# Performance work log

Measured on AMD Instinct MI355X. Metric: run time of the kernel, lower is better.

## Reference

```python
import jax, jax.numpy as jnp
import numpy as np
from jax import lax

# Model dims (match init_kwargs config)
HID = 2048      # hidden_size
NH = 64         # num_heads
P = 64          # head_dim
N = 128         # ssm_state_size
G = 1           # n_groups
CS = 256        # chunk_size
K = 4           # conv kernel
D_INNER = NH * P                  # 4096
CONV_DIM = D_INNER + 2 * G * N    # 4352
PROJ = D_INNER + CONV_DIM + NH    # 8512
EPS = 1e-5
BATCH, SEQ = 2, 2048


def setup_inputs() -> dict:
    key = jax.random.key(0)
    ks = jax.random.split(key, 8)
    hidden_states = jax.random.normal(ks[0], (BATCH, SEQ, HID), dtype=jnp.float32)
    W_in = jax.random.normal(ks[1], (PROJ, HID), dtype=jnp.float32) * 0.02
    conv_w = jax.random.normal(ks[2], (CONV_DIM, 1, K), dtype=jnp.float32) * 0.2
    conv_b = jax.random.normal(ks[3], (CONV_DIM,), dtype=jnp.float32) * 0.02
    # dt_bias initialized like inv-softplus of dt in [1e-3, 1e-1]
    dt = jnp.exp(jax.random.uniform(ks[4], (NH,)) * (np.log(0.1) - np.log(0.001)) + np.log(0.001))
    dt_bias = (dt + jnp.log(-jnp.expm1(-dt))).astype(jnp.float32)
    A_log = jnp.log(jnp.arange(1, NH + 1, dtype=jnp.float32))
    D_param = jnp.ones((NH,), dtype=jnp.float32)
    norm_w = jnp.ones((D_INNER,), dtype=jnp.float32)
    W_out = jax.random.normal(ks[5], (HID, D_INNER), dtype=jnp.float32) * 0.02
    return {"hidden_states": hidden_states, "W_in": W_in, "conv_w": conv_w,
            "conv_b": conv_b, "dt_bias": dt_bias, "A_log": A_log,
            "D_param": D_param, "norm_w": norm_w, "W_out": W_out}


def _segsum(x):
    # x: (..., c) -> (..., c, c); seg[i, j] = sum_{j < k <= i} x_k (diag 0), -inf above diag
    T = x.shape[-1]
    xc = jnp.cumsum(x, axis=-1)
    seg = xc[..., :, None] - xc[..., None, :]
    mask = jnp.tril(jnp.ones((T, T), dtype=bool))
    return jnp.where(mask, seg, -jnp.inf)


def _mamba2_forward(hidden_states, W_in, conv_w, conv_b, dt_bias, A_log, D_param, norm_w, W_out):
    B_, L_ = hidden_states.shape[:2]
    proj = hidden_states @ W_in.T                           # (b, l, PROJ)
    z = proj[..., :D_INNER]                                 # gate
    xBC = proj[..., D_INNER:D_INNER + CONV_DIM]
    dt = proj[..., D_INNER + CONV_DIM:]                     # (b, l, NH)

    # depthwise causal conv1d + silu
    xc = lax.conv_general_dilated(
        jnp.transpose(xBC, (0, 2, 1)), conv_w,
        window_strides=(1,), padding=[(K - 1, 0)],
        feature_group_count=CONV_DIM)                        # (b, CONV_DIM, l)
    xc = xc + conv_b[None, :, None]
    xBC = jax.nn.silu(jnp.transpose(xc, (0, 2, 1)))          # (b, l, CONV_DIM)

    x = xBC[..., :D_INNER].reshape(B_, L_, NH, P)
    Bm = xBC[..., D_INNER:D_INNER + G * N].reshape(B_, L_, G, N)
    Cm = xBC[..., D_INNER + G * N:].reshape(B_, L_, G, N)

    dt = jax.nn.softplus(dt + dt_bias)                       # (b, l, NH)
    A = -jnp.exp(A_log)                                      # (NH,)

    Bh = jnp.repeat(Bm, NH // G, axis=2)                     # (b, l, h, n)
    Ch = jnp.repeat(Cm, NH // G, axis=2)

    # ---- chunked SSD scan ----
    nc = L_ // CS
    x_dt = (x * dt[..., None]).reshape(B_, nc, CS, NH, P)    # (b, c, s, h, p)
    B_c = Bh.reshape(B_, nc, CS, NH, N)
    C_c = Ch.reshape(B_, nc, CS, NH, N)
    dA = jnp.transpose((dt * A).reshape(B_, nc, CS, NH), (0, 3, 1, 2))  # (b, h, c, s)
    A_cum = jnp.cumsum(dA, axis=-1)                          # (b, h, c, s)

    Lmat = jnp.exp(_segsum(dA))                              # (b, h, c, s, s)
    Y_diag = jnp.einsum('bclhn,bcshn,bhcls,bcshp->bclhp', C_c, B_c, Lmat, x_dt)

    decay_states = jnp.exp(A_cum[..., -1:] - A_cum)          # (b, h, c, s)
    states = jnp.einsum('bclhn,bhcl,bclhp->bchpn', B_c, decay_states, x_dt)

    da_last = A_cum[..., -1]                                 # (b, h, c)

    def step(prev, inp):
        s_k, d_k = inp                                       # (b,h,p,n), (b,h)
        new = prev * jnp.exp(d_k)[..., None, None] + s_k
        return new, prev

    _, prev_states = lax.scan(step, jnp.zeros((B_, NH, P, N), dtype=x.dtype),
                              (jnp.transpose(states, (1, 0, 2, 3, 4)),
                               jnp.transpose(da_last, (2, 0, 1))))
    prev_states = jnp.transpose(prev_states, (1, 2, 0, 3, 4))  # (b, h, c, p, n)

    Y_off = jnp.einsum('bclhn,bhcpn,bhcl->bclhp', C_c, prev_states, jnp.exp(A_cum))

    y = (Y_diag + Y_off).reshape(B_, L_, NH, P) + D_param[None, None, :, None] * x
    y = y.reshape(B_, L_, D_INNER)

    # gated grouped RMSNorm (norm_before_gate=False): norm(y * silu(z)) * w
    g = y * jax.nn.silu(z)
    gs = D_INNER // G
    gr = g.reshape(B_, L_, G, gs)
    var = jnp.mean(gr * gr, axis=-1, keepdims=True)
    gn = (gr * lax.rsqrt(var + EPS)).reshape(B_, L_, D_INNER) * norm_w

    return gn @ W_out.T                                      # (b, l, HID)


def reference(hidden_states, W_in, conv_w, conv_b, dt_bias, A_log, D_param, norm_w, W_out):
    return _mamba2_forward(hidden_states, W_in, conv_w, conv_b, dt_bias, A_log, D_param, norm_w, W_out)
```

## Files before the change

### kernel.cpp

```cpp
#include <hip/hip_runtime.h>

#define SEQLEN 2048
#define NHEADS 64
#define PDIM 64
#define NSTATE 128
#define CSIZE 256
#define NCHUNK 8
#define DINNER 4096
#define CONVD 4352
#define PROJD 8512

using s8v = __attribute__((ext_vector_type(8))) short;
using f4v = __attribute__((ext_vector_type(4))) float;
using bf8v = __attribute__((ext_vector_type(8))) __bf16;

__device__ __forceinline__ short f2bf(float x) {
  union { float f; unsigned u; } t; t.f = x;
  unsigned r = t.u + 0x7FFFu + ((t.u >> 16) & 1u);
  return (short)(r >> 16);
}
__device__ __forceinline__ float bf2f(short s) {
  union { unsigned u; float f; } t;
  t.u = ((unsigned)(unsigned short)s) << 16;
  return t.f;
}

__device__ __forceinline__ f4v mfma_bf16(s8v a, s8v b, f4v c) {
  return __builtin_amdgcn_mfma_f32_16x16x32_bf16(
      __builtin_bit_cast(bf8v, a), __builtin_bit_cast(bf8v, b), c, 0, 0, 0);
}

__device__ __forceinline__ void gll16(const void* g, void* l) {
  __builtin_amdgcn_global_load_lds(
      (const __attribute__((address_space(1))) unsigned*)g,
      (__attribute__((address_space(3))) unsigned*)l, 16, 0, 0);
}

__global__ __launch_bounds__(256) void cast_bf16_kernel(
    const float* __restrict__ in, short* __restrict__ out, int n4) {
  int i = blockIdx.x * 256 + threadIdx.x;
  if (i < n4) {
    float4 v = ((const float4*)in)[i];
    short4 o;
    o.x = f2bf(v.x); o.y = f2bf(v.y); o.z = f2bf(v.z); o.w = f2bf(v.w);
    ((short4*)out)[i] = o;
  }
}

__global__ __launch_bounds__(256, 4) void gemm1_kernel(
    const short* __restrict__ A, const short* __restrict__ B,
    short* __restrict__ z, short* __restrict__ xbc, float* __restrict__ dtb) {
  const int K = 2048;
  const int bid = blockIdx.x;
  const int panel = bid / (67 * 4), rem = bid % (67 * 4);
  const int bx = rem >> 2, by = panel * 4 + (rem & 3);
  const int tn0 = bx * 128, tm0 = by * 128;
  __shared__ alignas(16) short lds[8704];
  short* As = lds;
  short* Bs = lds + 4096;
  short* Cs = lds;
  const int tid = threadIdx.x;
  const int lane = tid & 63, wid = tid >> 6;
  const int wm = (wid >> 1) * 64, wn = (wid & 1) * 64;
  const int lr = lane & 15, q = lane >> 4;
  const int fA = (lr & 3) ^ ((lr >> 2) & 3);
  const int qs = (q ^ fA) * 8;
  f4v acc[4][4];
  for (int i = 0; i < 4; i++)
    for (int j = 0; j < 4; j++)
      for (int r = 0; r < 4; r++) acc[i][j][r] = 0.f;

  for (int k0 = 0; k0 < K; k0 += 32) {
    __syncthreads();
    for (int it = 0; it < 2; it++) {
      int ci = it * 256 + tid;
      int row = ci >> 2;
      int cg = ((ci & 3) ^ (row & 3) ^ ((row >> 2) & 3)) << 3;
      gll16(&A[(size_t)(tm0 + row) * K + k0 + cg], &As[ci * 8]);
      gll16(&B[(size_t)(tn0 + row) * K + k0 + cg], &Bs[ci * 8]);
    }
    __syncthreads();
    s8v af[4], bfr[4];
    for (int i = 0; i < 4; i++) af[i]  = *(const s8v*)&As[(wm + i * 16 + lr) * 32 + qs];
    for (int j = 0; j < 4; j++) bfr[j] = *(const s8v*)&Bs[(wn + j * 16 + lr) * 32 + qs];
    for (int i = 0; i < 4; i++)
      for (int j = 0; j < 4; j++)
        acc[i][j] = mfma_bf16(af[i], bfr[j], acc[i][j]);
  }
  __syncthreads();

  if (tn0 < 8448) {
    short* outp; int rowstride, colbase;
    if (tn0 < DINNER) { outp = z;   rowstride = DINNER; colbase = tn0; }
    else              { outp = xbc; rowstride = CONVD;  colbase = tn0 - DINNER; }
    for (int hh = 0; hh < 2; hh++) {
      if ((wid >> 1) == hh) {
        for (int i = 0; i < 4; i++)
          for (int j = 0; j < 4; j++)
            for (int r = 0; r < 4; r++)
              Cs[(i * 16 + q * 4 + r) * 136 + wn + j * 16 + lr] = f2bf(acc[i][j][r]);
      }
      __syncthreads();
      for (int ps = 0; ps < 4; ps++) {
        int idx = ps * 256 + tid;
        int r = idx >> 4, c8 = (idx & 15) * 8;
        s8v v = *(const s8v*)&Cs[r * 136 + c8];
        *(s8v*)&outp[(size_t)(tm0 + hh * 64 + r) * rowstride + colbase + c8] = v;
      }
      __syncthreads();
    }
  } else {
    for (int i = 0; i < 4; i++)
      for (int j = 0; j < 4; j++) {
        int c0 = tn0 + wn + j * 16 + lr;
        if (c0 < PROJD)
          for (int r = 0; r < 4; r++)
            dtb[(size_t)(tm0 + wm + i * 16 + q * 4 + r) * NHEADS + (c0 - 8448)] =
                acc[i][j][r];
      }
  }
}

__global__ __launch_bounds__(256, 4) void gemm_nt_bf16(
    const short* __restrict__ A, const short* __restrict__ B,
    float* __restrict__ C, int M, int N, int K) {
  const int nbx = N >> 7;
  const int bid = blockIdx.x;
  const int panel = bid / (nbx * 4), rem = bid % (nbx * 4);
  const int bx = rem >> 2, by = panel * 4 + (rem & 3);
  const int tn0 = bx * 128, tm0 = by * 128;
  __shared__ alignas(16) short As[128 * 32];
  __shared__ alignas(16) short Bs[128 * 32];
  const int tid = threadIdx.x;
  const int lane = tid & 63, wid = tid >> 6;
  const int wm = (wid >> 1) * 64, wn = (wid & 1) * 64;
  const int lr = lane & 15, q = lane >> 4;
  const int fA = (lr & 3) ^ ((lr >> 2) & 3);
  const int qs = (q ^ fA) * 8;
  f4v acc[4][4];
  for (int i = 0; i < 4; i++)
    for (int j = 0; j < 4; j++)
      for (int r = 0; r < 4; r++) acc[i][j][r] = 0.f;

  for (int k0 = 0; k0 < K; k0 += 32) {
    __syncthreads();
    for (int it = 0; it < 2; it++) {
      int ci = it * 256 + tid;
      int row = ci >> 2;
      int cg = ((ci & 3) ^ (row & 3) ^ ((row >> 2) & 3)) << 3;
      gll16(&A[(size_t)(tm0 + row) * K + k0 + cg], &As[ci * 8]);
      gll16(&B[(size_t)(tn0 + row) * K + k0 + cg], &Bs[ci * 8]);
    }
    __syncthreads();
    s8v af[4], bfr[4];
    for (int i = 0; i < 4; i++) af[i]  = *(const s8v*)&As[(wm + i * 16 + lr) * 32 + qs];
    for (int j = 0; j < 4; j++) bfr[j] = *(const s8v*)&Bs[(wn + j * 16 + lr) * 32 + qs];
    for (int i = 0; i < 4; i++)
      for (int j = 0; j < 4; j++)
        acc[i][j] = mfma_bf16(af[i], bfr[j], acc[i][j]);
  }
  for (int i = 0; i < 4; i++)
    for (int j = 0; j < 4; j++) {
      int r0 = tm0 + wm + i * 16 + q * 4;
      int c0 = tn0 + wn + j * 16 + lr;
      for (int r = 0; r < 4; r++)
        C[(size_t)(r0 + r) * N + c0] = acc[i][j][r];
    }
}

__global__ __launch_bounds__(256) void conv_silu_kernel(
    const short* __restrict__ xbc, const float* __restrict__ conv_w,
    const float* __restrict__ conv_b, short* __restrict__ xBCc) {
  int cc = blockIdx.x * 256 + threadIdx.x;
  int bl = blockIdx.y;
  int b = bl >> 11, l = bl & 2047;
  float4 wv = *(const float4*)&conv_w[cc * 4];
  float wk[4] = {wv.x, wv.y, wv.z, wv.w};
  float acc = conv_b[cc];
  const short* pbase = xbc + (size_t)(b * SEQLEN) * CONVD + cc;
#pragma unroll
  for (int k = 0; k < 4; k++) {
    int ls = l - 3 + k;
    if (ls >= 0) acc += bf2f(pbase[(size_t)ls * CONVD]) * wk[k];
  }
  float sv = acc / (1.f + expf(-acc));
  xBCc[(size_t)bl * CONVD + cc] = f2bf(sv);
}

__global__ __launch_bounds__(256) void dt_kernel(
    float* __restrict__ dtb, const float* __restrict__ dt_bias) {
  int idx = blockIdx.x * 256 + threadIdx.x;
  int hh = idx & 63;
  float v = dtb[idx] + dt_bias[hh];
  dtb[idx] = (v > 20.f) ? v : log1pf(expf(v));
}

__global__ __launch_bounds__(256) void ssd_states_kernel(
    const short* __restrict__ xBCc, const float* __restrict__ dtp,
    const float* __restrict__ A_log, short* __restrict__ states,
    float* __restrict__ da_last) {
  const int blk = blockIdx.x;
  const int h = blk & 63, cc = (blk >> 6) & 7, b = blk >> 9;
  const int tid = threadIdx.x;
  __shared__ float dt_s[CSIZE], Acum[CSIZE], w_s[CSIZE];
  __shared__ float xw[64][64];
  __shared__ float Bt[64][NSTATE];
  const size_t row0 = (size_t)(b * SEQLEN + cc * CSIZE);
  dt_s[tid] = dtp[(row0 + tid) * NHEADS + h];
  __syncthreads();
  if (tid == 0) {
    float Aval = -expf(A_log[h]);
    float s = 0.f;
    for (int i = 0; i < CSIZE; i++) { s += dt_s[i]; Acum[i] = s * Aval; }
    da_last[(size_t)(b * NHEADS + h) * NCHUNK + cc] = Acum[CSIZE - 1];
  }
  __syncthreads();
  float total = Acum[CSIZE - 1];
  w_s[tid] = dt_s[tid] * expf(total - Acum[tid]);
  float acc[4][8];
  for (int a = 0; a < 4; a++) for (int j = 0; j < 8; j++) acc[a][j] = 0.f;
  const int pi = (tid & 15) * 4, ni = (tid >> 4) * 8;
  for (int lt = 0; lt < 4; lt++) {
    __syncthreads();
    for (int i = 0; i < 4; i++) {
      int idx = tid + i * 256;
      int r = idx >> 4, c4 = (idx & 15) << 2;
      short4 v = *(const short4*)&xBCc[(row0 + lt * 64 + r) * CONVD + h * PDIM + c4];
      float wl = w_s[lt * 64 + r];
      xw[r][c4 + 0] = bf2f(v.x) * wl;
      xw[r][c4 + 1] = bf2f(v.y) * wl;
      xw[r][c4 + 2] = bf2f(v.z) * wl;
      xw[r][c4 + 3] = bf2f(v.w) * wl;
    }
    for (int i = 0; i < 8; i++) {
      int idx = tid + i * 256;
      int r = idx >> 5, c4 = (idx & 31) << 2;
      short4 v = *(const short4*)&xBCc[(row0 + lt * 64 + r) * CONVD + DINNER + c4];
      Bt[r][c4 + 0] = bf2f(v.x);
      Bt[r][c4 + 1] = bf2f(v.y);
      Bt[r][c4 + 2] = bf2f(v.z);
      Bt[r][c4 + 3] = bf2f(v.w);
    }
    __syncthreads();
    for (int l = 0; l < 64; l++) {
      float4 xv = *(const float4*)&xw[l][pi];
      float4 b0 = *(const float4*)&Bt[l][ni];
      float4 b1 = *(const float4*)&Bt[l][ni + 4];
      float xa[4] = {xv.x, xv.y, xv.z, xv.w};
      float bb[8] = {b0.x, b0.y, b0.z, b0.w, b1.x, b1.y, b1.z, b1.w};
      for (int a = 0; a < 4; a++)
        for (int j = 0; j < 8; j++)
          acc[a][j] += xa[a] * bb[j];
    }
  }
  const size_t sbase = (((size_t)b * NCHUNK + cc) * NHEADS + h) * (PDIM * NSTATE);
  for (int a = 0; a < 4; a++) {
    short o[8];
    for (int j = 0; j < 8; j++) o[j] = f2bf(acc[a][j]);
    *(s8v*)&states[sbase + (size_t)(pi + a) * NSTATE + ni] = *(const s8v*)o;
  }
}

__global__ __launch_bounds__(256) void scan_kernel(
    short* __restrict__ states, const float* __restrict__ da_last) {
  const int bh = blockIdx.x >> 2, sl = blockIdx.x & 3;
  const int b = bh >> 6, h = bh & 63;
  const int tid = threadIdx.x;
  float prev[8];
  for (int i = 0; i < 8; i++) prev[i] = 0.f;
  for (int c = 0; c < NCHUNK; c++) {
    const size_t base = (((size_t)b * NCHUNK + c) * NHEADS + h) * (PDIM * NSTATE)
                      + sl * 2048;
    const float d = expf(da_last[(size_t)bh * NCHUNK + c]);
    for (int i = 0; i < 8; i++) {
      size_t e = base + tid + i * 256;
      float s = bf2f(states[e]);
      states[e] = f2bf(prev[i]);
      prev[i] = prev[i] * d + s;
    }
  }
}

__global__ __launch_bounds__(256) void ssd_y_kernel(
    const short* __restrict__ xBCc, const float* __restrict__ dtp,
    const float* __restrict__ A_log, const float* __restrict__ D_param,
    const short* __restrict__ prevs, short* __restrict__ y) {
  const int blk = blockIdx.x;
  const int h = blk & 63, cc = (blk >> 6) & 7, b = blk >> 9;
  const int tid = threadIdx.x;
  const int lane = tid & 63, w = tid >> 6;
  const int lr = lane & 15, q = lane >> 4;
  __shared__ float dt_s[CSIZE];
  __shared__ float Acum[CSIZE];
  __shared__ short C_s[64][136];
  __shared__ short BP_s[64][136];
  __shared__ short xdtT[64][72];
  __shared__ short Mt[64][72];
  const size_t row0 = (size_t)(b * SEQLEN + cc * CSIZE);
  dt_s[tid] = dtp[(row0 + tid) * NHEADS + h];
  __syncthreads();
  if (tid == 0) {
    float Aval = -expf(A_log[h]);
    float s = 0.f;
    for (int i = 0; i < CSIZE; i++) { s += dt_s[i]; Acum[i] = s * Aval; }
  }
  const float Dh = D_param[h];
  const size_t prevbase = (((size_t)b * NCHUNK + cc) * NHEADS + h) * (PDIM * NSTATE);
  const int wl0 = w * 16;

  for (int lt = 0; lt < 4; lt++) {
    __syncthreads();
    for (int i = 0; i < 4; i++) {
      int idx = tid + i * 256;
      int r = idx >> 4, c8 = (idx & 15) << 3;
      *(s8v*)&C_s[r][c8] =
          *(const s8v*)&xBCc[(row0 + lt * 64 + r) * CONVD + DINNER + NSTATE + c8];
      *(s8v*)&BP_s[r][c8] = *(const s8v*)&prevs[prevbase + (size_t)r * NSTATE + c8];
    }
    __syncthreads();
    f4v acc[4];
    for (int j = 0; j < 4; j++) for (int r = 0; r < 4; r++) acc[j][r] = 0.f;
    for (int ks = 0; ks < 4; ks++) {
      s8v a = *(const s8v*)&C_s[wl0 + lr][ks * 32 + q * 8];
      for (int j = 0; j < 4; j++) {
        s8v bb = *(const s8v*)&BP_s[j * 16 + lr][ks * 32 + q * 8];
        acc[j] = mfma_bf16(a, bb, acc[j]);
      }
    }
    for (int r = 0; r < 4; r++) {
      float e = __expf(Acum[lt * 64 + wl0 + q * 4 + r]);
      for (int j = 0; j < 4; j++) acc[j][r] *= e;
    }
    for (int st = 0; st <= lt; st++) {
      __syncthreads();
      for (int i = 0; i < 4; i++) {
        int idx = tid + i * 256;
        int r = idx >> 4, c8 = (idx & 15) << 3;
        *(s8v*)&BP_s[r][c8] =
            *(const s8v*)&xBCc[(row0 + st * 64 + r) * CONVD + DINNER + c8];
      }
      for (int i = 0; i < 4; i++) {
        int idx = tid + i * 256;
        int r = idx >> 4, c4 = (idx & 15) << 2;
        float dtv = dt_s[st * 64 + r];
        short4 v = *(const short4*)&xBCc[(row0 + st * 64 + r) * CONVD + h * PDIM + c4];
        xdtT[c4 + 0][r] = f2bf(bf2f(v.x) * dtv);
        xdtT[c4 + 1][r] = f2bf(bf2f(v.y) * dtv);
        xdtT[c4 + 2][r] = f2bf(bf2f(v.z) * dtv);
        xdtT[c4 + 3][r] = f2bf(bf2f(v.w) * dtv);
      }
      __syncthreads();
      f4v sacc[4];
      for (int j = 0; j < 4; j++) for (int r = 0; r < 4; r++) sacc[j][r] = 0.f;
      for (int ks = 0; ks < 4; ks++) {
        s8v a = *(const s8v*)&C_s[wl0 + lr][ks * 32 + q * 8];
        for (int j = 0; j < 4; j++) {
          s8v bb = *(const s8v*)&BP_s[j * 16 + lr][ks * 32 + q * 8];
          sacc[j] = mfma_bf16(a, bb, sacc[j]);
        }
      }
      int lbase = lt * 64 + wl0 + q * 4;
      for (int j = 0; j < 4; j++) {
        int sg = st * 64 + j * 16 + lr;
        for (int r = 0; r < 4; r++) {
          int ll = lbase + r;
          float m = (sg <= ll) ? sacc[j][r] * __expf(Acum[ll] - Acum[sg]) : 0.f;
          Mt[wl0 + q * 4 + r][j * 16 + lr] = f2bf(m);
        }
      }
      __syncthreads();
      for (int ss2 = 0; ss2 < 2; ss2++) {
        s8v a = *(const s8v*)&Mt[wl0 + lr][ss2 * 32 + q * 8];
        for (int j = 0; j < 4; j++) {
          s8v bb = *(const s8v*)&xdtT[j * 16 + lr][ss2 * 32 + q * 8];
          acc[j] = mfma_bf16(a, bb, acc[j]);
        }
      }
    }
    for (int j = 0; j < 4; j++)
      for (int r = 0; r < 4; r++) {
        int lrow = wl0 + q * 4 + r;
        int ll = lt * 64 + lrow;
        int p = j * 16 + lr;
        float xv = bf2f(xBCc[(row0 + ll) * CONVD + h * PDIM + p]);
        Mt[lrow][p] = f2bf(acc[j][r] + Dh * xv);
      }
    __syncthreads();
    for (int ps = 0; ps < 2; ps++) {
      int r = ps * 32 + (tid >> 3);
      int c8 = (tid & 7) * 8;
      s8v v = *(const s8v*)&Mt[r][c8];
      *(s8v*)&y[(row0 + lt * 64 + r) * DINNER + h * PDIM + c8] = v;
    }
  }
}

__global__ __launch_bounds__(256) void norm_kernel(
    const short* __restrict__ y, const short* __restrict__ z,
    const float* __restrict__ norm_w, short* __restrict__ g) {
  int bl = blockIdx.x, tid = threadIdx.x;
  const short4* yrow = (const short4*)(y + (size_t)bl * DINNER);
  const short4* zrow = (const short4*)(z + (size_t)bl * DINNER);
  float gv[16];
  float ss = 0.f;
  for (int i = 0; i < 4; i++) {
    short4 yv = yrow[tid + i * 256];
    short4 zv = zrow[tid + i * 256];
    float zf[4] = {bf2f(zv.x), bf2f(zv.y), bf2f(zv.z), bf2f(zv.w)};
    float yf[4] = {bf2f(yv.x), bf2f(yv.y), bf2f(yv.z), bf2f(yv.w)};
    for (int t = 0; t < 4; t++) {
      float gg = yf[t] * (zf[t] / (1.f + expf(-zf[t])));
      gv[i * 4 + t] = gg;
      ss += gg * gg;
    }
  }
  for (int off = 32; off > 0; off >>= 1) ss += __shfl_down(ss, off);
  __shared__ float red[4];
  __shared__ float rsS;
  if ((tid & 63) == 0) red[tid >> 6] = ss;
  __syncthreads();
  if (tid == 0) rsS = rsqrtf((red[0] + red[1] + red[2] + red[3]) * (1.f / 4096.f) + 1e-5f);
  __syncthreads();
  float rs = rsS;
  for (int i = 0; i < 4; i++) {
    int j4 = (tid + i * 256) * 4;
    float4 nw = *(const float4*)&norm_w[j4];
    short4 o;
    o.x = f2bf(gv[i * 4 + 0] * rs * nw.x);
    o.y = f2bf(gv[i * 4 + 1] * rs * nw.y);
    o.z = f2bf(gv[i * 4 + 2] * rs * nw.z);
    o.w = f2bf(gv[i * 4 + 3] * rs * nw.w);
    *(short4*)&g[(size_t)bl * DINNER + j4] = o;
  }
}

extern "C" void kernel_launch(void* const* d_in, const int* in_sizes, int n_in,
                              void* d_out, int out_size, void* d_ws, size_t ws_size,
                              hipStream_t stream) {
  const float* hidden  = (const float*)d_in[0];
  const float* W_in    = (const float*)d_in[1];
  const float* conv_w  = (const float*)d_in[2];
  const float* conv_b  = (const float*)d_in[3];
  const float* dt_bias = (const float*)d_in[4];
  const float* A_log   = (const float*)d_in[5];
  const float* D_param = (const float*)d_in[6];
  const float* norm_w  = (const float*)d_in[7];
  const float* W_out   = (const float*)d_in[8];
  float* out = (float*)d_out;

  char* ws = (char*)d_ws;
  short* z_bf  = (short*)(ws + 0);
  float* dtb   = (float*)(ws + 33554432);
  float* da_l  = (float*)(ws + 34603008);
  short* xbc_pre = (short*)(ws + 34607104);
  short* y_bf    = (short*)(ws + 34607104);
  short* hid_bf  = (short*)(ws + 70258688);
  short* win_bf  = (short*)(ws + 87035904);
  short* xBCc    = (short*)(ws + 70258688);
  short* states  = (short*)(ws + 105910272);
  short* g_bf    = (short*)(ws + 70258688);
  short* wout_bf = (short*)(ws + 105910272);
  if (ws_size < (size_t)122687488) return;

  cast_bf16_kernel<<<8192, 256, 0, stream>>>(hidden, hid_bf, 2097152);
  cast_bf16_kernel<<<17024, 256, 0, stream>>>(W_in, win_bf, 4358144);

  gemm1_kernel<<<2144, 256, 0, stream>>>(hid_bf, win_bf, z_bf, xbc_pre, dtb);

  conv_silu_kernel<<<dim3(17, 4096), 256, 0, stream>>>(xbc_pre, conv_w, conv_b, xBCc);
  dt_kernel<<<1024, 256, 0, stream>>>(dtb, dt_bias);

  ssd_states_kernel<<<1024, 256, 0, stream>>>(xBCc, dtb, A_log, states, da_l);
  scan_kernel<<<512, 256, 0, stream>>>(states, da_l);
  ssd_y_kernel<<<1024, 256, 0, stream>>>(xBCc, dtb, A_log, D_param, states, y_bf);

  norm_kernel<<<4096, 256, 0, stream>>>(y_bf, z_bf, norm_w, g_bf);
  cast_bf16_kernel<<<8192, 256, 0, stream>>>(W_out, wout_bf, 2097152);

  gemm_nt_bf16<<<512, 256, 0, stream>>>(g_bf, wout_bf, out, 4096, 2048, 4096);
}
```

Before: 689.3 us.

## Rewrite input projection GEMM with 256x256 tiles and pipelined LDS staging

Replaces the 128x128 input-projection GEMM with a 256x256-tile, 512-thread kernel that uses a 64-wide K step. A and B tiles are double-buffered through global_load_lds, and the next stages load in phases interleaved with MFMA groups using explicit waitcnt, barriers and setprio. Block IDs are remapped across the 8 XCDs, and the output GEMM gets the same XCD-aware block swizzle. The goal is more data reuse per tile, better latency hiding and better L2 locality, at the cost of large LDS use and register pressure that limit occupancy to about 2 blocks.

```diff
diff --git a/kernel.cpp b/kernel.cpp
--- a/kernel.cpp
+++ b/kernel.cpp
@@ -47,77 +47,162 @@
   }
 }
 
-__global__ __launch_bounds__(256, 4) void gemm1_kernel(
+
+#define G1_STAGE_A(dst, h, kt) do {                                          \
+    _Pragma("unroll")                                                        \
+    for (int it_ = 0; it_ < 2; ++it_) {                                      \
+      int ci_ = it_ * 512 + tid;                                             \
+      int r_ = ci_ >> 3;                                                     \
+      int g_ = ((ci_ & 7) ^ (r_ & 7)) << 3;                                  \
+      gll16(&A[(size_t)(tm0 + (h) * 128 + r_) * 2048 + (kt) * 64 + g_],      \
+            &(dst)[(h) * 8192 + ci_ * 8]);                                   \
+    }                                                                        \
+  } while (0)
+
+#define G1_STAGE_B(dst, h, kt) do {                                          \
+    _Pragma("unroll")                                                        \
+    for (int it_ = 0; it_ < 2; ++it_) {                                      \
+      int ci_ = it_ * 512 + tid;                                             \
+      int r_ = ci_ >> 3;                                                     \
+      int g_ = ((ci_ & 7) ^ (r_ & 7)) << 3;                                  \
+      int br_ = tn0 + (h) * 128 + r_;                                        \
+      if (br_ > 8511) br_ = 8511;       \
+      gll16(&B[(size_t)br_ * 2048 + (kt) * 64 + g_],                         \
+            &(dst)[(h) * 8192 + ci_ * 8]);                                   \
+    }                                                                        \
+  } while (0)
+
+#define RD_A(m, ks) \
+  (*(const s8v*)&Ad[(wm + (m) * 16 + lr) * 64 + (((ks) * 4 + q) ^ sw7) * 8])
+#define RD_B(n, ks) \
+  (*(const s8v*)&Bd[(wn + (n) * 16 + lr) * 64 + (((ks) * 4 + q) ^ sw7) * 8])
+
+#define G1_PHASE(m0, STAGE_STMT) do {                                        \
+    s8v a00 = RD_A(m0, 0), a01 = RD_A(m0, 1);                                \
+    s8v a10 = RD_A((m0) + 1, 0), a11 = RD_A((m0) + 1, 1);                    \
+    STAGE_STMT;                                                              \
+    __builtin_amdgcn_s_barrier();                                            \
+    asm volatile("s_waitcnt lgkmcnt(0)" ::: "memory");                       \
+    __builtin_amdgcn_s_setprio(1);                                           \
+    _Pragma("unroll") for (int n = 0; n < 4; ++n)                            \
+      acc[m0][n] = mfma_bf16(a00, bk0[n], acc[m0][n]);                       \
+    _Pragma("unroll") for (int n = 0; n < 4; ++n)                            \
+      acc[m0][n] = mfma_bf16(a01, bk1[n], acc[m0][n]);                       \
+    _Pragma("unroll") for (int n = 0; n < 4; ++n)                            \
+      acc[(m0) + 1][n] = mfma_bf16(a10, bk0[n], acc[(m0) + 1][n]);           \
+    _Pragma("unroll") for (int n = 0; n < 4; ++n)                            \
+      acc[(m0) + 1][n] = mfma_bf16(a11, bk1[n], acc[(m0) + 1][n]);           \
+    __builtin_amdgcn_s_setprio(0);                                           \
+    __builtin_amdgcn_s_barrier();                                            \
+  } while (0)
+
+__global__ __launch_bounds__(512, 2) void gemm1_256(
     const short* __restrict__ A, const short* __restrict__ B,
     short* __restrict__ z, short* __restrict__ xbc, float* __restrict__ dtb) {
-  const int K = 2048;
+  const int NT = 32;
   const int bid = blockIdx.x;
-  const int panel = bid / (67 * 4), rem = bid % (67 * 4);
+  const int sid = (bid & 7) * 68 + (bid >> 3);
+  const int panel = sid / 136, rem = sid % 136;
   const int bx = rem >> 2, by = panel * 4 + (rem & 3);
-  const int tn0 = bx * 128, tm0 = by * 128;
-  __shared__ alignas(16) short lds[8704];
-  short* As = lds;
-  short* Bs = lds + 4096;
-  short* Cs = lds;
+  const int tm0 = by * 256, tn0 = bx * 256;
+  __shared__ alignas(16) short lds[65536];
   const int tid = threadIdx.x;
   const int lane = tid & 63, wid = tid >> 6;
-  const int wm = (wid >> 1) * 64, wn = (wid & 1) * 64;
+  const int wm = (wid >> 2) * 128, wn = (wid & 3) * 64;
   const int lr = lane & 15, q = lane >> 4;
-  const int fA = (lr & 3) ^ ((lr >> 2) & 3);
-  const int qs = (q ^ fA) * 8;
-  f4v acc[4][4];
-  for (int i = 0; i < 4; i++)
-    for (int j = 0; j < 4; j++)
-      for (int r = 0; r < 4; r++) acc[i][j][r] = 0.f;
-
-  for (int k0 = 0; k0 < K; k0 += 32) {
-    __syncthreads();
-    for (int it = 0; it < 2; it++) {
-      int ci = it * 256 + tid;
-      int row = ci >> 2;
-      int cg = ((ci & 3) ^ (row & 3) ^ ((row >> 2) & 3)) << 3;
-      gll16(&A[(size_t)(tm0 + row) * K + k0 + cg], &As[ci * 8]);
-      gll16(&B[(size_t)(tn0 + row) * K + k0 + cg], &Bs[ci * 8]);
-    }
-    __syncthreads();
-    s8v af[4], bfr[4];
-    for (int i = 0; i < 4; i++) af[i]  = *(const s8v*)&As[(wm + i * 16 + lr) * 32 + qs];
-    for (int j = 0; j < 4; j++) bfr[j] = *(const s8v*)&Bs[(wn + j * 16 + lr) * 32 + qs];
-    for (int i = 0; i < 4; i++)
-      for (int j = 0; j < 4; j++)
-        acc[i][j] = mfma_bf16(af[i], bfr[j], acc[i][j]);
-  }
-  __syncthreads();
-
-  if (tn0 < 8448) {
-    short* outp; int rowstride, colbase;
-    if (tn0 < DINNER) { outp = z;   rowstride = DINNER; colbase = tn0; }
-    else              { outp = xbc; rowstride = CONVD;  colbase = tn0 - DINNER; }
-    for (int hh = 0; hh < 2; hh++) {
-      if ((wid >> 1) == hh) {
-        for (int i = 0; i < 4; i++)
-          for (int j = 0; j < 4; j++)
-            for (int r = 0; r < 4; r++)
-              Cs[(i * 16 + q * 4 + r) * 136 + wn + j * 16 + lr] = f2bf(acc[i][j][r]);
-      }
-      __syncthreads();
-      for (int ps = 0; ps < 4; ps++) {
-        int idx = ps * 256 + tid;
-        int r = idx >> 4, c8 = (idx & 15) * 8;
-        s8v v = *(const s8v*)&Cs[r * 136 + c8];
-        *(s8v*)&outp[(size_t)(tm0 + hh * 64 + r) * rowstride + colbase + c8] = v;
-      }
-      __syncthreads();
-    }
-  } else {
-    for (int i = 0; i < 4; i++)
-      for (int j = 0; j < 4; j++) {
-        int c0 = tn0 + wn + j * 16 + lr;
-        if (c0 < PROJD)
-          for (int r = 0; r < 4; r++)
-            dtb[(size_t)(tm0 + wm + i * 16 + q * 4 + r) * NHEADS + (c0 - 8448)] =
-                acc[i][j][r];
-      }
+  const int sw7 = lr & 7;
+
+  f4v acc[8][4];
+#pragma unroll
+  for (int m = 0; m < 8; ++m)
+#pragma unroll
+    for (int n = 0; n < 4; ++n)
+#pragma unroll
+      for (int r = 0; r < 4; ++r) acc[m][n][r] = 0.f;
+
+  {
+    short* A0 = lds;
+    short* B0 = lds + 16384;
+    short* B1 = lds + 49152;
+    G1_STAGE_A(A0, 0, 0); G1_STAGE_A(A0, 1, 0);
+    G1_STAGE_B(B0, 0, 0); G1_STAGE_B(B0, 1, 0);
+    G1_STAGE_B(B1, 0, 1); G1_STAGE_B(B1, 1, 1);
+  }
+
+  for (int t = 0; t < NT; ++t) {
+    short* Ad = lds + ((t & 1) << 15);
+    short* Bd = Ad + 16384;
+    short* An = lds + (((t + 1) & 1) << 15);
+    s8v bk0[4], bk1[4];
+    if (t + 1 < NT) {
+      G1_STAGE_A(An, 0, t + 1);
+      asm volatile("s_waitcnt vmcnt(6)" ::: "memory");
+    } else {
+      asm volatile("s_waitcnt vmcnt(0)" ::: "memory");
+    }
+    __builtin_amdgcn_s_barrier();
+#pragma unroll
+    for (int n = 0; n < 4; ++n) { bk0[n] = RD_B(n, 0); bk1[n] = RD_B(n, 1); }
+    {
+      s8v a00 = RD_A(0, 0), a01 = RD_A(0, 1);
+      s8v a10 = RD_A(1, 0), a11 = RD_A(1, 1);
+      __builtin_amdgcn_s_setprio(1);
+#pragma unroll
+      for (int n = 0; n < 4; ++n) acc[0][n] = mfma_bf16(a00, bk0[n], acc[0][n]);
+#pragma unroll
+      for (int n = 0; n < 4; ++n) acc[0][n] = mfma_bf16(a01, bk1[n], acc[0][n]);
+#pragma unroll
+      for (int n = 0; n < 4; ++n) acc[1][n] = mfma_bf16(a10, bk0[n], acc[1][n]);
+#pragma unroll
+      for (int n = 0; n < 4; ++n) acc[1][n] = mfma_bf16(a11, bk1[n], acc[1][n]);
+      __builtin_amdgcn_s_setprio(0);
+    }
+    __builtin_amdgcn_s_barrier();
+    G1_PHASE(2, if (t + 1 < NT) G1_STAGE_A(An, 1, t + 1));
+    G1_PHASE(4, if (t + 2 < NT) G1_STAGE_B(Bd, 0, t + 2));
+    G1_PHASE(6, if (t + 2 < NT) G1_STAGE_B(Bd, 1, t + 2));
+  }
+
+  if (bx == 33) {
+    if (wn == 0) {
+#pragma unroll
+      for (int m = 0; m < 8; ++m)
+#pragma unroll
+        for (int n = 0; n < 4; ++n) {
+          int col = n * 16 + lr;
+#pragma unroll
+          for (int r = 0; r < 4; ++r) {
+            int row = tm0 + wm + m * 16 + q * 4 + r;
+            dtb[(size_t)row * NHEADS + col] = acc[m][n][r];
+          }
+        }
+    }
+    return;
+  }
+  short* outp; int stride, colbase;
+  if (bx < 16) { outp = z;   stride = DINNER; colbase = tn0; }
+  else         { outp = xbc; stride = CONVD;  colbase = tn0 - DINNER; }
+  short* Cs = lds;
+  for (int h = 0; h < 2; ++h) {
+    __syncthreads();
+    if ((wid >> 2) == h) {
+#pragma unroll
+      for (int m = 0; m < 8; ++m)
+#pragma unroll
+        for (int n = 0; n < 4; ++n)
+#pragma unroll
+          for (int r = 0; r < 4; ++r)
+            Cs[(m * 16 + q * 4 + r) * 264 + wn + n * 16 + lr] =
+                f2bf(acc[m][n][r]);
+    }
+    __syncthreads();
+#pragma unroll
+    for (int itr = 0; itr < 8; ++itr) {
+      int idx = itr * 512 + tid;
+      int r = idx >> 5, c8 = (idx & 31) * 8;
+      s8v v = *(const s8v*)&Cs[r * 264 + c8];
+      *(s8v*)&outp[(size_t)(tm0 + h * 128 + r) * stride + colbase + c8] = v;
+    }
   }
 }
 
@@ -125,7 +210,8 @@
     const short* __restrict__ A, const short* __restrict__ B,
     float* __restrict__ C, int M, int N, int K) {
   const int nbx = N >> 7;
-  const int bid = blockIdx.x;
+  const int bid0 = blockIdx.x;
+  const int bid = (bid0 & 7) * (gridDim.x >> 3) + (bid0 >> 3);
   const int panel = bid / (nbx * 4), rem = bid % (nbx * 4);
   const int bx = rem >> 2, by = panel * 4 + (rem & 3);
   const int tn0 = bx * 128, tm0 = by * 128;
@@ -465,7 +551,7 @@
   cast_bf16_kernel<<<8192, 256, 0, stream>>>(hidden, hid_bf, 2097152);
   cast_bf16_kernel<<<17024, 256, 0, stream>>>(W_in, win_bf, 4358144);
 
-  gemm1_kernel<<<2144, 256, 0, stream>>>(hid_bf, win_bf, z_bf, xbc_pre, dtb);
+  gemm1_256<<<544, 512, 0, stream>>>(hid_bf, win_bf, z_bf, xbc_pre, dtb);
 
   conv_silu_kernel<<<dim3(17, 4096), 256, 0, stream>>>(xbc_pre, conv_w, conv_b, xBCc);
   dt_kernel<<<1024, 256, 0, stream>>>(dtb, dt_bias);
```

Measured after the change: 665.1 us. 1.04x faster.
